# Performance work log

Hardware: AMD Instinct MI355X
Metric: run time of the kernel (lower is better)

## Reference

```python
import jax, jax.numpy as jnp
import numpy as np

N = 100000   # nodes
E = 1600000  # edges (before self-loops)
F = 128      # num_features
H = 128      # hidden_dim
EPS = 1e-5   # BatchNorm eps


def setup_inputs() -> dict:
    key = jax.random.key(0)
    ks = jax.random.split(key, 8)
    x = jax.random.normal(ks[0], (N, F), dtype=jnp.float32)
    edge_index = jax.random.randint(ks[1], (2, E), 0, N, dtype=jnp.int64)

    def lin(k, din, dout):
        s = 1.0 / np.sqrt(din)
        kw, kb = jax.random.split(k)
        W = jax.random.uniform(kw, (din, dout), jnp.float32, -s, s)
        b = jax.random.uniform(kb, (dout,), jnp.float32, -s, s)
        return W, b

    W1, b1 = lin(ks[2], F, H)
    W2, b2 = lin(ks[3], H, H)
    W3, b3 = lin(ks[4], H, H)
    Wc, bc = lin(ks[5], H, 2)

    def bn_params():
        return (jnp.ones((H,), jnp.float32), jnp.zeros((H,), jnp.float32),
                jnp.zeros((H,), jnp.float32), jnp.ones((H,), jnp.float32))

    g1, be1, rm1, rv1 = bn_params()
    g2, be2, rm2, rv2 = bn_params()
    g3, be3, rm3, rv3 = bn_params()

    return {"x": x, "edge_index": edge_index,
            "W1": W1, "b1": b1, "W2": W2, "b2": b2, "W3": W3, "b3": b3,
            "g1": g1, "be1": be1, "rm1": rm1, "rv1": rv1,
            "g2": g2, "be2": be2, "rm2": rm2, "rv2": rv2,
            "g3": g3, "be3": be3, "rm3": rm3, "rv3": rv3,
            "Wc": Wc, "bc": bc}


def _gcn_norm(edge_index, num_nodes):
    # add self-loops, compute symmetric normalization (PyG GCNConv default)
    loop = jnp.arange(num_nodes, dtype=edge_index.dtype)
    src = jnp.concatenate([edge_index[0], loop])
    dst = jnp.concatenate([edge_index[1], loop])
    deg = jax.ops.segment_sum(jnp.ones_like(dst, dtype=jnp.float32), dst,
                              num_segments=num_nodes)
    dinv = jnp.where(deg > 0, jax.lax.rsqrt(deg), 0.0)
    norm = dinv[src] * dinv[dst]  # [E+N]
    return src, dst, norm


def _gcn_conv(x, W, b, src, dst, norm, num_nodes):
    h = x @ W                              # [N, H] linear first
    msg = h[src] * norm[:, None]           # gather + scale  [E+N, H]
    out = jax.ops.segment_sum(msg, dst, num_segments=num_nodes)  # scatter-add
    return out + b


def _bn_eval(x, g, be, rm, rv):
    return (x - rm) * jax.lax.rsqrt(rv + EPS) * g + be


def reference(x, edge_index,
              W1, b1, W2, b2, W3, b3,
              g1, be1, rm1, rv1,
              g2, be2, rm2, rv2,
              g3, be3, rm3, rv3,
              Wc, bc):
    n = x.shape[0]
    src, dst, norm = _gcn_norm(edge_index, n)
    h = _gcn_conv(x, W1, b1, src, dst, norm, n)
    h = _bn_eval(jax.nn.relu(h), g1, be1, rm1, rv1)
    # dropout: identity in eval mode
    h = _gcn_conv(h, W2, b2, src, dst, norm, n)
    h = _bn_eval(jax.nn.relu(h), g2, be2, rm2, rv2)
    h = _gcn_conv(h, W3, b3, src, dst, norm, n)
    h = _bn_eval(jax.nn.relu(h), g3, be3, rm3, rv3)
    return h @ Wc + bc  # [N, 2]
```

## Files before the change

kernel.cpp:

```cpp
#include <hip/hip_runtime.h>
#include <hip/hip_fp16.h>

#define BN_EPS 1e-5f
#define CHUNK 4096
#define BBITS 7

typedef _Float16 half8 __attribute__((ext_vector_type(8)));
typedef float f32x4 __attribute__((ext_vector_type(4)));

__device__ __forceinline__ float4 f4zero() { return make_float4(0.f, 0.f, 0.f, 0.f); }


__global__ __launch_bounds__(256) void k_pack_hist(const float* __restrict__ W1,
                                                   const float* __restrict__ W2,
                                                   const float* __restrict__ W3,
                                                   _Float16* __restrict__ pW,
                                                   const int* __restrict__ dst,
                                                   int* __restrict__ tableT,
                                                   int nA, int nbuck, int e) {
    __shared__ int h[1024];
    int tid = threadIdx.x;
    if (blockIdx.x < 24) {
        int t = blockIdx.x * 256 + tid;
        int wi = t >> 11;
        int tt = t & 2047;
        const float* W = (wi == 0) ? W1 : ((wi == 1) ? W2 : W3);
        int kc = tt >> 9;
        int rem = tt & 511;
        int ct = rem >> 6;
        int lane = rem & 63;
        int q = lane >> 4;
        int col = ct * 16 + (lane & 15);
        half8 hh;
#pragma unroll
        for (int j = 0; j < 8; ++j)
            hh[j] = (_Float16)W[(kc * 32 + q * 8 + j) * 128 + col];
        *(half8*)(pW + (size_t)t * 8) = hh;
        return;
    }
    int blk = blockIdx.x - 24;
    for (int k = tid; k < 1024; k += 256) h[k] = 0;
    __syncthreads();
    int base = blk * CHUNK;
    if (base + CHUNK <= e && (e & 3) == 0) {
        const int4* d4 = (const int4*)(dst + base);
#pragma unroll
        for (int t = 0; t < CHUNK / 1024; ++t) {
            int4 d = d4[t * 256 + tid];
            atomicAdd(&h[d.x >> BBITS], 1);
            atomicAdd(&h[d.y >> BBITS], 1);
            atomicAdd(&h[d.z >> BBITS], 1);
            atomicAdd(&h[d.w >> BBITS], 1);
        }
    } else {
        for (int i = base + tid; i < e && i < base + CHUNK; i += 256)
            atomicAdd(&h[dst[i] >> BBITS], 1);
    }
    __syncthreads();
    for (int k = tid; k < nbuck; k += 256)
        tableT[(size_t)k * nA + blk] = h[k];
}


__global__ __launch_bounds__(1024) void k_scan_block(const int* __restrict__ in,
                                                     int* __restrict__ outp,
                                                     int* __restrict__ partials, int len) {
    __shared__ int s[1024];
    int t = threadIdx.x;
    int gid = blockIdx.x * 1024 + t;
    int v = (gid < len) ? in[gid] : 0;
    int x = v;
    s[t] = x;
    __syncthreads();
    for (int d = 1; d < 1024; d <<= 1) {
        int y = (t >= d) ? s[t - d] : 0;
        __syncthreads();
        x += y;
        s[t] = x;
        __syncthreads();
    }
    if (gid < len) outp[gid] = x - v;
    if (t == 1023) partials[blockIdx.x] = x;
}

__global__ __launch_bounds__(256) void k_scan_addp(int* __restrict__ data,
                                                   const int* __restrict__ partials, int len) {
    __shared__ int red[256];
    int tid = threadIdx.x;
    int K = blockIdx.x >> 2;
    int s = 0;
    for (int t = tid; t < K; t += 256) s += partials[t];
    red[tid] = s;
    __syncthreads();
    for (int d = 128; d > 0; d >>= 1) {
        if (tid < d) red[tid] += red[tid + d];
        __syncthreads();
    }
    int gid = blockIdx.x * 256 + tid;
    if (gid < len) data[gid] += red[0];
}


__global__ __launch_bounds__(256) void k_bucket_scatter(const int* __restrict__ src,
                                                        const int* __restrict__ dst,
                                                        const int* __restrict__ tableT,
                                                        int2* __restrict__ bed,
                                                        int nA, int nbuck, int e) {
    __shared__ int cur[1024];
    int blk = blockIdx.x, tid = threadIdx.x;
    for (int k = tid; k < nbuck; k += 256)
        cur[k] = tableT[(size_t)k * nA + blk];
    __syncthreads();
    int base = blk * CHUNK;
    if (base + CHUNK <= e && (e & 3) == 0) {
        const int4* s4 = (const int4*)(src + base);
        const int4* d4 = (const int4*)(dst + base);
#pragma unroll
        for (int t = 0; t < CHUNK / 1024; ++t) {
            int4 s = s4[t * 256 + tid];
            int4 d = d4[t * 256 + tid];
            int p0 = atomicAdd(&cur[d.x >> BBITS], 1); bed[p0] = make_int2(s.x, d.x);
            int p1 = atomicAdd(&cur[d.y >> BBITS], 1); bed[p1] = make_int2(s.y, d.y);
            int p2 = atomicAdd(&cur[d.z >> BBITS], 1); bed[p2] = make_int2(s.z, d.z);
            int p3 = atomicAdd(&cur[d.w >> BBITS], 1); bed[p3] = make_int2(s.w, d.w);
        }
    } else {
        for (int i = base + tid; i < e && i < base + CHUNK; i += 256) {
            int d = dst[i];
            int p = atomicAdd(&cur[d >> BBITS], 1);
            bed[p] = make_int2(src[i], d);
        }
    }
}


__global__ __launch_bounds__(256) void k_bucket_rank(const int2* __restrict__ bed,
                                                     const int* __restrict__ tableT,
                                                     int* __restrict__ brank,
                                                     int* __restrict__ counts,
                                                     float* __restrict__ dinv,
                                                     int* __restrict__ localOff,
                                                     int* __restrict__ btot,
                                                     int nA, int nbuck, int n, int e) {
    __shared__ int lcnt[128];
    __shared__ int lscan[128];
    int b = blockIdx.x, tid = threadIdx.x;
    if (tid < 128) lcnt[tid] = 0;
    __syncthreads();
    int start = tableT[(size_t)b * nA];
    int end = (b + 1 < nbuck) ? tableT[(size_t)(b + 1) * nA] : e;
    for (int i = start + tid; i < end; i += 256) {
        int2 q = bed[i];
        brank[i] = atomicAdd(&lcnt[q.y & 127], 1);
    }
    __syncthreads();
    int padded = 0;
    if (tid < 128) {
        padded = (lcnt[tid] + 7) & ~7;
        lscan[tid] = padded;
    }
    __syncthreads();
    for (int d = 1; d < 128; d <<= 1) {
        int y = (tid < 128 && tid >= d) ? lscan[tid - d] : 0;
        __syncthreads();
        if (tid < 128) lscan[tid] += y;
        __syncthreads();
    }
    if (tid < 128) {
        int node = (b << BBITS) + tid;
        if (node < n) {
            int c = lcnt[tid];
            counts[node] = c;
            dinv[node] = rsqrtf((float)(c + 1));
            localOff[node] = lscan[tid] - padded;
        }
        if (tid == 127) btot[b] = lscan[127];
    }
}


__global__ __launch_bounds__(1024) void k_scan_buckets(const int* __restrict__ btot,
                                                       int* __restrict__ bucketBase, int nbuck) {
    __shared__ int s[1024];
    int t = threadIdx.x;
    int v = (t < nbuck) ? btot[t] : 0;
    int x = v;
    s[t] = x;
    __syncthreads();
    for (int d = 1; d < 1024; d <<= 1) {
        int y = (t >= d) ? s[t - d] : 0;
        __syncthreads();
        x += y;
        s[t] = x;
        __syncthreads();
    }
    if (t < nbuck) bucketBase[t] = x - v;
    if (t == nbuck - 1) bucketBase[nbuck] = x;
}


__global__ __launch_bounds__(256) void k_finalize(const int* __restrict__ counts,
                                                  const int* __restrict__ localOff,
                                                  const int* __restrict__ bucketBase,
                                                  int* __restrict__ offs,
                                                  int* __restrict__ er,
                                                  const int2* __restrict__ bed,
                                                  const int* __restrict__ brank,
                                                  unsigned int* __restrict__ bufAzero,
                                                  int n, int e, int gN, int nbuck) {
    int tid = threadIdx.x;
    if (blockIdx.x < gN) {
        int node = blockIdx.x * 256 + tid;
        if (node < n) {
            int c = counts[node];
            int o = bucketBase[node >> BBITS] + localOff[node];
            offs[node] = o;
            int pc = (c + 7) & ~7;
            for (int j = c; j < pc; ++j) er[o + j] = n << 8;
        }
        if (node == 0) offs[n] = bucketBase[nbuck];
        if (blockIdx.x == 0 && tid < 64) bufAzero[tid] = 0u;
    } else {
        int i = ((blockIdx.x - gN) * 256 + tid) * 2;
        if (i + 1 < e) {
            int4 q = *(const int4*)(bed + i);
            int2 r = *(const int2*)(brank + i);
            er[bucketBase[q.y >> BBITS] + localOff[q.y] + r.x] = q.x << 8;
            er[bucketBase[q.w >> BBITS] + localOff[q.w] + r.y] = q.z << 8;
        } else if (i < e) {
            int2 q = bed[i];
            er[bucketBase[q.y >> BBITS] + localOff[q.y] + brank[i]] = q.x << 8;
        }
    }
}


template <bool AF32>
__global__ __launch_bounds__(256) void k_gemm_mfma(const void* __restrict__ Av,
                                                   const _Float16* __restrict__ pW,
                                                   const float* __restrict__ dinv,
                                                   uint4* __restrict__ C, int n) {
    __shared__ char smem[32768];
    uint4* sW = (uint4*)smem;
    int tid = threadIdx.x;

    {
        const uint4* gW = (const uint4*)pW;
#pragma unroll
        for (int i = 0; i < 8; ++i) sW[tid + 256 * i] = gW[tid + 256 * i];
    }
    __syncthreads();

    int wave = tid >> 6, lane = tid & 63;
    int quad = lane >> 4, l16 = lane & 15;
    int row0 = blockIdx.x * 64 + wave * 16;
    int arow = row0 + l16;
    int arowc = (arow < n) ? arow : (n - 1);

    half8 af[4];
    if (AF32) {
        const float* A = (const float*)Av + (size_t)arowc * 128 + quad * 8;
#pragma unroll
        for (int kc = 0; kc < 4; ++kc) {
            float4 lo = *(const float4*)(A + kc * 32);
            float4 hi = *(const float4*)(A + kc * 32 + 4);
            half8 h;
            h[0] = (_Float16)lo.x; h[1] = (_Float16)lo.y;
            h[2] = (_Float16)lo.z; h[3] = (_Float16)lo.w;
            h[4] = (_Float16)hi.x; h[5] = (_Float16)hi.y;
            h[6] = (_Float16)hi.z; h[7] = (_Float16)hi.w;
            af[kc] = h;
        }
    } else {
        const _Float16* A = (const _Float16*)Av + (size_t)arowc * 128 + quad * 8;
#pragma unroll
        for (int kc = 0; kc < 4; ++kc)
            af[kc] = *(const half8*)(A + kc * 32);
    }

    f32x4 acc[8];
#pragma unroll
    for (int ct = 0; ct < 8; ++ct) acc[ct] = (f32x4){0.f, 0.f, 0.f, 0.f};

#pragma unroll
    for (int kc = 0; kc < 4; ++kc) {
#pragma unroll
        for (int ct = 0; ct < 8; ++ct) {
            half8 bf = *(half8*)&sW[(kc * 8 + ct) * 64 + lane];
            acc[ct] = __builtin_amdgcn_mfma_f32_16x16x32_f16(af[kc], bf, acc[ct], 0, 0, 0);
        }
    }

    __syncthreads();

    _Float16* eb = (_Float16*)smem + wave * 16 * 136;
    float dv[4];
#pragma unroll
    for (int r = 0; r < 4; ++r) {
        int rr = row0 + quad * 4 + r;
        dv[r] = dinv[(rr < n) ? rr : (n - 1)];
    }
#pragma unroll
    for (int ct = 0; ct < 8; ++ct)
#pragma unroll
        for (int r = 0; r < 4; ++r)
            eb[(quad * 4 + r) * 136 + ct * 16 + l16] = (_Float16)(acc[ct][r] * dv[r]);

#pragma unroll
    for (int i = 0; i < 4; ++i) {
        int linear = i * 64 + lane;
        int r = linear >> 4, c = linear & 15;
        uint4 v = *(uint4*)((char*)eb + r * 272 + c * 16);
        int row = row0 + r;
        if (row < n) C[(size_t)row * 16 + c] = v;
    }
}


__device__ __forceinline__ void acc_row(float4& acc, uint2 q) {
    asm("v_fma_mix_f32 %0, %1, 1.0, %0 op_sel:[0,0,0] op_sel_hi:[1,0,0]" : "+v"(acc.x) : "v"(q.x));
    asm("v_fma_mix_f32 %0, %1, 1.0, %0 op_sel:[1,0,0] op_sel_hi:[1,0,0]" : "+v"(acc.y) : "v"(q.x));
    asm("v_fma_mix_f32 %0, %1, 1.0, %0 op_sel:[0,0,0] op_sel_hi:[1,0,0]" : "+v"(acc.z) : "v"(q.y));
    asm("v_fma_mix_f32 %0, %1, 1.0, %0 op_sel:[1,0,0] op_sel_hi:[1,0,0]" : "+v"(acc.w) : "v"(q.y));
}

template <bool FUSE_CLS>
__global__ __launch_bounds__(256) void k_aggregate(const uint2* __restrict__ Ah,
                                                   const int* __restrict__ offs,
                                                   const int* __restrict__ er,
                                                   const float* __restrict__ dinv,
                                                   const float* __restrict__ bias,
                                                   const float* __restrict__ g,
                                                   const float* __restrict__ be,
                                                   const float* __restrict__ rm,
                                                   const float* __restrict__ rv,
                                                   uint2* __restrict__ Hout,
                                                   const float* __restrict__ Wc,
                                                   const float* __restrict__ bc,
                                                   float* __restrict__ out, int n) {
    int lane = threadIdx.x & 31;
    int node = blockIdx.x * 8 + (threadIdx.x >> 5);
    if (node >= n) return;

    const char* AhB = (const char*)Ah;
    unsigned int l8 = (unsigned int)lane * 8u;

    float4 acc = f4zero();
    acc_row(acc, *(const uint2*)(AhB + (((unsigned int)node << 8) + l8)));

    int e0 = offs[node], e1 = offs[node + 1];
    for (int e = e0; e < e1; e += 8) {
        int4 ra = *(const int4*)(er + e);
        int4 rb = *(const int4*)(er + e + 4);
        uint2 v0 = *(const uint2*)(AhB + ((unsigned int)ra.x + l8));
        uint2 v1 = *(const uint2*)(AhB + ((unsigned int)ra.y + l8));
        uint2 v2 = *(const uint2*)(AhB + ((unsigned int)ra.z + l8));
        uint2 v3 = *(const uint2*)(AhB + ((unsigned int)ra.w + l8));
        uint2 v4 = *(const uint2*)(AhB + ((unsigned int)rb.x + l8));
        uint2 v5 = *(const uint2*)(AhB + ((unsigned int)rb.y + l8));
        uint2 v6 = *(const uint2*)(AhB + ((unsigned int)rb.z + l8));
        uint2 v7 = *(const uint2*)(AhB + ((unsigned int)rb.w + l8));
        acc_row(acc, v0); acc_row(acc, v1); acc_row(acc, v2); acc_row(acc, v3);
        acc_row(acc, v4); acc_row(acc, v5); acc_row(acc, v6); acc_row(acc, v7);
    }

    float di = dinv[node];
    acc.x *= di; acc.y *= di; acc.z *= di; acc.w *= di;

    float4 b4  = ((const float4*)bias)[lane];
    float4 g4  = ((const float4*)g)[lane];
    float4 be4 = ((const float4*)be)[lane];
    float4 rm4 = ((const float4*)rm)[lane];
    float4 rv4 = ((const float4*)rv)[lane];

    float4 o;
    float v;
    v = fmaxf(acc.x + b4.x, 0.f); o.x = (v - rm4.x) * rsqrtf(rv4.x + BN_EPS) * g4.x + be4.x;
    v = fmaxf(acc.y + b4.y, 0.f); o.y = (v - rm4.y) * rsqrtf(rv4.y + BN_EPS) * g4.y + be4.y;
    v = fmaxf(acc.z + b4.z, 0.f); o.z = (v - rm4.z) * rsqrtf(rv4.z + BN_EPS) * g4.z + be4.z;
    v = fmaxf(acc.w + b4.w, 0.f); o.w = (v - rm4.w) * rsqrtf(rv4.w + BN_EPS) * g4.w + be4.w;

    if (!FUSE_CLS) {
        __half2 p0 = __floats2half2_rn(o.x, o.y);
        __half2 p1 = __floats2half2_rn(o.z, o.w);
        uint2 u;
        u.x = *(unsigned int*)&p0;
        u.y = *(unsigned int*)&p1;
        Hout[(size_t)node * 32 + lane] = u;
    } else {
        const float4* Wv = (const float4*)Wc;
        float4 w01 = Wv[2 * lane];
        float4 w23 = Wv[2 * lane + 1];
        float p0 = o.x * w01.x + o.y * w01.z + o.z * w23.x + o.w * w23.z;
        float p1 = o.x * w01.y + o.y * w01.w + o.z * w23.y + o.w * w23.w;
#pragma unroll
        for (int d = 16; d >= 1; d >>= 1) {
            p0 += __shfl_down(p0, d, 32);
            p1 += __shfl_down(p1, d, 32);
        }
        if (lane == 0) {
            out[node * 2 + 0] = p0 + bc[0];
            out[node * 2 + 1] = p1 + bc[1];
        }
    }
}


extern "C" void kernel_launch(void* const* d_in, const int* in_sizes, int n_in,
                              void* d_out, int out_size, void* d_ws, size_t ws_size,
                              hipStream_t stream) {
    const float* x   = (const float*)d_in[0];
    const int*   ei  = (const int*)d_in[1];
    const float* W1  = (const float*)d_in[2];
    const float* b1  = (const float*)d_in[3];
    const float* W2  = (const float*)d_in[4];
    const float* b2  = (const float*)d_in[5];
    const float* W3  = (const float*)d_in[6];
    const float* b3  = (const float*)d_in[7];
    const float* g1  = (const float*)d_in[8];
    const float* be1 = (const float*)d_in[9];
    const float* rm1 = (const float*)d_in[10];
    const float* rv1 = (const float*)d_in[11];
    const float* g2  = (const float*)d_in[12];
    const float* be2 = (const float*)d_in[13];
    const float* rm2 = (const float*)d_in[14];
    const float* rv2 = (const float*)d_in[15];
    const float* g3  = (const float*)d_in[16];
    const float* be3 = (const float*)d_in[17];
    const float* rm3 = (const float*)d_in[18];
    const float* rv3 = (const float*)d_in[19];
    const float* Wc  = (const float*)d_in[20];
    const float* bc  = (const float*)d_in[21];
    float* out = (float*)d_out;

    int n = in_sizes[0] / 128;
    int e = in_sizes[1] / 2;
    const int* src = ei;
    const int* dst = ei + e;

    char* ws = (char*)d_ws;
    size_t off = 0;
    auto alloc = [&](size_t bytes) -> char* {
        char* p = ws + off;
        off += (bytes + 255) & ~(size_t)255;
        return p;
    };
    int nA    = (e + CHUNK - 1) / CHUNK;
    int nbuck = (n + (1 << BBITS) - 1) >> BBITS;
    int tlen  = nbuck * nA;
    int erCap = e + 8 * n;

    char*      bufA     = (char*) alloc((size_t)(n + 1) * 256);
    char*      bufH     = (char*) alloc((size_t)n * 256);
    float*     dinv     = (float*)alloc((size_t)n * 4);
    int*       counts   = (int*)  alloc((size_t)n * 4);
    int*       offs     = (int*)  alloc((size_t)(n + 1) * 4);
    int*       localOff = (int*)  alloc((size_t)n * 4);
    int*       btot     = (int*)  alloc((size_t)(nbuck + 1) * 4);
    int*       bktBase  = (int*)  alloc((size_t)(nbuck + 1) * 4);
    int*       tableT   = (int*)  alloc((size_t)(tlen + 1) * 4);
    int*       parts    = (int*)  alloc(8192);
    int*       er       = (int*)  alloc((size_t)erCap * 4);
    _Float16*  pW       = (_Float16*)alloc(3 * 16384 * 2);
    (void)ws_size; (void)n_in; (void)out_size;

    int2* bed   = (int2*)bufH;
    int*  brank = (int*)(bufH + (size_t)e * 8);

    int gN  = (n + 255) / 256;
    int nbT = (tlen + 1023) / 1024;

    k_pack_hist<<<24 + nA, 256, 0, stream>>>(W1, W2, W3, pW, dst, tableT, nA, nbuck, e);
    k_scan_block<<<nbT, 1024, 0, stream>>>(tableT, tableT, parts, tlen);
    k_scan_addp<<<(tlen + 255) / 256, 256, 0, stream>>>(tableT, parts, tlen);
    k_bucket_scatter<<<nA, 256, 0, stream>>>(src, dst, tableT, bed, nA, nbuck, e);
    k_bucket_rank<<<nbuck, 256, 0, stream>>>(bed, tableT, brank, counts, dinv, localOff,
                                             btot, nA, nbuck, n, e);
    k_scan_buckets<<<1, 1024, 0, stream>>>(btot, bktBase, nbuck);
    int gP = gN + (e / 2 + 255) / 256 + 1;
    k_finalize<<<gP, 256, 0, stream>>>(counts, localOff, bktBase, offs, er, bed, brank,
                                       (unsigned int*)(bufA + (size_t)n * 256), n, e, gN, nbuck);

    int gGemm = (n + 63) / 64;
    int gAgg  = (n + 7) / 8;

    k_gemm_mfma<true><<<gGemm, 256, 0, stream>>>(x, pW, dinv, (uint4*)bufA, n);
    k_aggregate<false><<<gAgg, 256, 0, stream>>>((const uint2*)bufA, offs, er, dinv,
                                                 b1, g1, be1, rm1, rv1, (uint2*)bufH,
                                                 nullptr, nullptr, nullptr, n);

    k_gemm_mfma<false><<<gGemm, 256, 0, stream>>>(bufH, pW + 16384, dinv, (uint4*)bufA, n);
    k_aggregate<false><<<gAgg, 256, 0, stream>>>((const uint2*)bufA, offs, er, dinv,
                                                 b2, g2, be2, rm2, rv2, (uint2*)bufH,
                                                 nullptr, nullptr, nullptr, n);

    k_gemm_mfma<false><<<gGemm, 256, 0, stream>>>(bufH, pW + 32768, dinv, (uint4*)bufA, n);
    k_aggregate<true><<<gAgg, 256, 0, stream>>>((const uint2*)bufA, offs, er, dinv,
                                                b3, g3, be3, rm3, rv3, nullptr,
                                                Wc, bc, out, n);
}
```

Baseline: 395.4 us.

## Fuse bucket scan into first GEMM launch and widen aggregate loads to 16 bytes

The single-block bucket-base scan is merged into the first-layer GEMM launch: block 0 does the scan with 256 threads, each handling a serial chunk, and the remaining blocks run the fp32-input GEMM. This removes one launch and lets the scan overlap with GEMM work. The aggregation kernel now uses 16 lanes per node with 16-byte gathers instead of 32 lanes with 8-byte gathers, so fewer, wider memory requests are issued per edge. The per-thread scan buffer has a fixed size of 8, so it assumes nbuck is at most 2048, and the half-width groups raise register use per thread.

```diff
diff --git a/kernel.cpp b/kernel.cpp
--- a/kernel.cpp
+++ b/kernel.cpp
@@ -179,23 +179,132 @@
 }
 
 
-__global__ __launch_bounds__(1024) void k_scan_buckets(const int* __restrict__ btot,
-                                                       int* __restrict__ bucketBase, int nbuck) {
-    __shared__ int s[1024];
-    int t = threadIdx.x;
-    int v = (t < nbuck) ? btot[t] : 0;
-    int x = v;
-    s[t] = x;
-    __syncthreads();
-    for (int d = 1; d < 1024; d <<= 1) {
-        int y = (t >= d) ? s[t - d] : 0;
-        __syncthreads();
-        x += y;
-        s[t] = x;
-        __syncthreads();
-    }
-    if (t < nbuck) bucketBase[t] = x - v;
-    if (t == nbuck - 1) bucketBase[nbuck] = x;
+template <bool AF32>
+__device__ __forceinline__ void gemm_body(int bid, int tid, char* smem,
+                                          const void* __restrict__ Av,
+                                          const _Float16* __restrict__ pW,
+                                          const float* __restrict__ dinv,
+                                          uint4* __restrict__ C, int n) {
+    uint4* sW = (uint4*)smem;
+    {
+        const uint4* gW = (const uint4*)pW;
+#pragma unroll
+        for (int i = 0; i < 8; ++i) sW[tid + 256 * i] = gW[tid + 256 * i];
+    }
+    __syncthreads();
+
+    int wave = tid >> 6, lane = tid & 63;
+    int quad = lane >> 4, l16 = lane & 15;
+    int row0 = bid * 64 + wave * 16;
+    int arow = row0 + l16;
+    int arowc = (arow < n) ? arow : (n - 1);
+
+    half8 af[4];
+    if (AF32) {
+        const float* A = (const float*)Av + (size_t)arowc * 128 + quad * 8;
+#pragma unroll
+        for (int kc = 0; kc < 4; ++kc) {
+            float4 lo = *(const float4*)(A + kc * 32);
+            float4 hi = *(const float4*)(A + kc * 32 + 4);
+            half8 h;
+            h[0] = (_Float16)lo.x; h[1] = (_Float16)lo.y;
+            h[2] = (_Float16)lo.z; h[3] = (_Float16)lo.w;
+            h[4] = (_Float16)hi.x; h[5] = (_Float16)hi.y;
+            h[6] = (_Float16)hi.z; h[7] = (_Float16)hi.w;
+            af[kc] = h;
+        }
+    } else {
+        const _Float16* A = (const _Float16*)Av + (size_t)arowc * 128 + quad * 8;
+#pragma unroll
+        for (int kc = 0; kc < 4; ++kc)
+            af[kc] = *(const half8*)(A + kc * 32);
+    }
+
+    f32x4 acc[8];
+#pragma unroll
+    for (int ct = 0; ct < 8; ++ct) acc[ct] = (f32x4){0.f, 0.f, 0.f, 0.f};
+
+#pragma unroll
+    for (int kc = 0; kc < 4; ++kc) {
+#pragma unroll
+        for (int ct = 0; ct < 8; ++ct) {
+            half8 bf = *(half8*)&sW[(kc * 8 + ct) * 64 + lane];
+            acc[ct] = __builtin_amdgcn_mfma_f32_16x16x32_f16(af[kc], bf, acc[ct], 0, 0, 0);
+        }
+    }
+
+    __syncthreads();
+
+    _Float16* eb = (_Float16*)smem + wave * 16 * 136;
+    float dv[4];
+#pragma unroll
+    for (int r = 0; r < 4; ++r) {
+        int rr = row0 + quad * 4 + r;
+        dv[r] = dinv[(rr < n) ? rr : (n - 1)];
+    }
+#pragma unroll
+    for (int ct = 0; ct < 8; ++ct)
+#pragma unroll
+        for (int r = 0; r < 4; ++r)
+            eb[(quad * 4 + r) * 136 + ct * 16 + l16] = (_Float16)(acc[ct][r] * dv[r]);
+
+#pragma unroll
+    for (int i = 0; i < 4; ++i) {
+        int linear = i * 64 + lane;
+        int r = linear >> 4, c = linear & 15;
+        uint4 v = *(uint4*)((char*)eb + r * 272 + c * 16);
+        int row = row0 + r;
+        if (row < n) C[(size_t)row * 16 + c] = v;
+    }
+}
+
+__global__ __launch_bounds__(256) void k_gemm_mfma(const void* __restrict__ Av,
+                                                   const _Float16* __restrict__ pW,
+                                                   const float* __restrict__ dinv,
+                                                   uint4* __restrict__ C, int n) {
+    __shared__ char smem[32768];
+    gemm_body<false>(blockIdx.x, threadIdx.x, smem, Av, pW, dinv, C, n);
+}
+
+
+__global__ __launch_bounds__(256) void k_scanb_gemm(const int* __restrict__ btot,
+                                                    int* __restrict__ bucketBase, int nbuck,
+                                                    const float* __restrict__ x,
+                                                    const _Float16* __restrict__ pW,
+                                                    const float* __restrict__ dinv,
+                                                    uint4* __restrict__ C, int n) {
+    __shared__ char smem[32768];
+    int tid = threadIdx.x;
+    if (blockIdx.x > 0) {
+        gemm_body<true>(blockIdx.x - 1, tid, smem, x, pW, dinv, C, n);
+        return;
+    }
+    int* s = (int*)smem;
+    int per = (nbuck + 255) >> 8;
+    int base = tid * per;
+    int loc[8];
+    int sum = 0;
+#pragma unroll 4
+    for (int j = 0; j < per; ++j) {
+        int v = (base + j < nbuck) ? btot[base + j] : 0;
+        loc[j] = sum;
+        sum += v;
+    }
+    int x_ = sum;
+    s[tid] = x_;
+    __syncthreads();
+    for (int d = 1; d < 256; d <<= 1) {
+        int y = (tid >= d) ? s[tid - d] : 0;
+        __syncthreads();
+        x_ += y;
+        s[tid] = x_;
+        __syncthreads();
+    }
+    int off = x_ - sum;
+#pragma unroll 4
+    for (int j = 0; j < per; ++j)
+        if (base + j < nbuck) bucketBase[base + j] = off + loc[j];
+    if (tid == 255) bucketBase[nbuck] = x_;
 }
 
 
@@ -235,97 +344,20 @@
 }
 
 
-template <bool AF32>
-__global__ __launch_bounds__(256) void k_gemm_mfma(const void* __restrict__ Av,
-                                                   const _Float16* __restrict__ pW,
-                                                   const float* __restrict__ dinv,
-                                                   uint4* __restrict__ C, int n) {
-    __shared__ char smem[32768];
-    uint4* sW = (uint4*)smem;
-    int tid = threadIdx.x;
-
-    {
-        const uint4* gW = (const uint4*)pW;
-#pragma unroll
-        for (int i = 0; i < 8; ++i) sW[tid + 256 * i] = gW[tid + 256 * i];
-    }
-    __syncthreads();
-
-    int wave = tid >> 6, lane = tid & 63;
-    int quad = lane >> 4, l16 = lane & 15;
-    int row0 = blockIdx.x * 64 + wave * 16;
-    int arow = row0 + l16;
-    int arowc = (arow < n) ? arow : (n - 1);
-
-    half8 af[4];
-    if (AF32) {
-        const float* A = (const float*)Av + (size_t)arowc * 128 + quad * 8;
-#pragma unroll
-        for (int kc = 0; kc < 4; ++kc) {
-            float4 lo = *(const float4*)(A + kc * 32);
-            float4 hi = *(const float4*)(A + kc * 32 + 4);
-            half8 h;
-            h[0] = (_Float16)lo.x; h[1] = (_Float16)lo.y;
-            h[2] = (_Float16)lo.z; h[3] = (_Float16)lo.w;
-            h[4] = (_Float16)hi.x; h[5] = (_Float16)hi.y;
-            h[6] = (_Float16)hi.z; h[7] = (_Float16)hi.w;
-            af[kc] = h;
-        }
-    } else {
-        const _Float16* A = (const _Float16*)Av + (size_t)arowc * 128 + quad * 8;
-#pragma unroll
-        for (int kc = 0; kc < 4; ++kc)
-            af[kc] = *(const half8*)(A + kc * 32);
-    }
-
-    f32x4 acc[8];
-#pragma unroll
-    for (int ct = 0; ct < 8; ++ct) acc[ct] = (f32x4){0.f, 0.f, 0.f, 0.f};
-
-#pragma unroll
-    for (int kc = 0; kc < 4; ++kc) {
-#pragma unroll
-        for (int ct = 0; ct < 8; ++ct) {
-            half8 bf = *(half8*)&sW[(kc * 8 + ct) * 64 + lane];
-            acc[ct] = __builtin_amdgcn_mfma_f32_16x16x32_f16(af[kc], bf, acc[ct], 0, 0, 0);
-        }
-    }
-
-    __syncthreads();
-
-    _Float16* eb = (_Float16*)smem + wave * 16 * 136;
-    float dv[4];
-#pragma unroll
-    for (int r = 0; r < 4; ++r) {
-        int rr = row0 + quad * 4 + r;
-        dv[r] = dinv[(rr < n) ? rr : (n - 1)];
-    }
-#pragma unroll
-    for (int ct = 0; ct < 8; ++ct)
-#pragma unroll
-        for (int r = 0; r < 4; ++r)
-            eb[(quad * 4 + r) * 136 + ct * 16 + l16] = (_Float16)(acc[ct][r] * dv[r]);
-
-#pragma unroll
-    for (int i = 0; i < 4; ++i) {
-        int linear = i * 64 + lane;
-        int r = linear >> 4, c = linear & 15;
-        uint4 v = *(uint4*)((char*)eb + r * 272 + c * 16);
-        int row = row0 + r;
-        if (row < n) C[(size_t)row * 16 + c] = v;
-    }
-}
-
-
-__device__ __forceinline__ void acc_row(float4& acc, uint2 q) {
-    asm("v_fma_mix_f32 %0, %1, 1.0, %0 op_sel:[0,0,0] op_sel_hi:[1,0,0]" : "+v"(acc.x) : "v"(q.x));
-    asm("v_fma_mix_f32 %0, %1, 1.0, %0 op_sel:[1,0,0] op_sel_hi:[1,0,0]" : "+v"(acc.y) : "v"(q.x));
-    asm("v_fma_mix_f32 %0, %1, 1.0, %0 op_sel:[0,0,0] op_sel_hi:[1,0,0]" : "+v"(acc.z) : "v"(q.y));
-    asm("v_fma_mix_f32 %0, %1, 1.0, %0 op_sel:[1,0,0] op_sel_hi:[1,0,0]" : "+v"(acc.w) : "v"(q.y));
-}
+__device__ __forceinline__ void acc_row4(float4& aL, float4& aH, uint4 q) {
+    asm("v_fma_mix_f32 %0, %1, 1.0, %0 op_sel:[0,0,0] op_sel_hi:[1,0,0]" : "+v"(aL.x) : "v"(q.x));
+    asm("v_fma_mix_f32 %0, %1, 1.0, %0 op_sel:[1,0,0] op_sel_hi:[1,0,0]" : "+v"(aL.y) : "v"(q.x));
+    asm("v_fma_mix_f32 %0, %1, 1.0, %0 op_sel:[0,0,0] op_sel_hi:[1,0,0]" : "+v"(aL.z) : "v"(q.y));
+    asm("v_fma_mix_f32 %0, %1, 1.0, %0 op_sel:[1,0,0] op_sel_hi:[1,0,0]" : "+v"(aL.w) : "v"(q.y));
+    asm("v_fma_mix_f32 %0, %1, 1.0, %0 op_sel:[0,0,0] op_sel_hi:[1,0,0]" : "+v"(aH.x) : "v"(q.z));
+    asm("v_fma_mix_f32 %0, %1, 1.0, %0 op_sel:[1,0,0] op_sel_hi:[1,0,0]" : "+v"(aH.y) : "v"(q.z));
+    asm("v_fma_mix_f32 %0, %1, 1.0, %0 op_sel:[0,0,0] op_sel_hi:[1,0,0]" : "+v"(aH.z) : "v"(q.w));
+    asm("v_fma_mix_f32 %0, %1, 1.0, %0 op_sel:[1,0,0] op_sel_hi:[1,0,0]" : "+v"(aH.w) : "v"(q.w));
+}
+
 
 template <bool FUSE_CLS>
-__global__ __launch_bounds__(256) void k_aggregate(const uint2* __restrict__ Ah,
+__global__ __launch_bounds__(256) void k_aggregate(const uint4* __restrict__ Ah,
                                                    const int* __restrict__ offs,
                                                    const int* __restrict__ er,
                                                    const float* __restrict__ dinv,
@@ -334,69 +366,82 @@
                                                    const float* __restrict__ be,
                                                    const float* __restrict__ rm,
                                                    const float* __restrict__ rv,
-                                                   uint2* __restrict__ Hout,
+                                                   uint4* __restrict__ Hout,
                                                    const float* __restrict__ Wc,
                                                    const float* __restrict__ bc,
                                                    float* __restrict__ out, int n) {
-    int lane = threadIdx.x & 31;
-    int node = blockIdx.x * 8 + (threadIdx.x >> 5);
+    int lane = threadIdx.x & 15;
+    int node = blockIdx.x * 16 + (threadIdx.x >> 4);
     if (node >= n) return;
 
     const char* AhB = (const char*)Ah;
-    unsigned int l8 = (unsigned int)lane * 8u;
-
-    float4 acc = f4zero();
-    acc_row(acc, *(const uint2*)(AhB + (((unsigned int)node << 8) + l8)));
+    unsigned int l16 = (unsigned int)lane * 16u;
+
+    float4 aL = f4zero(), aH = f4zero();
+    acc_row4(aL, aH, *(const uint4*)(AhB + (((unsigned int)node << 8) + l16)));
 
     int e0 = offs[node], e1 = offs[node + 1];
     for (int e = e0; e < e1; e += 8) {
         int4 ra = *(const int4*)(er + e);
         int4 rb = *(const int4*)(er + e + 4);
-        uint2 v0 = *(const uint2*)(AhB + ((unsigned int)ra.x + l8));
-        uint2 v1 = *(const uint2*)(AhB + ((unsigned int)ra.y + l8));
-        uint2 v2 = *(const uint2*)(AhB + ((unsigned int)ra.z + l8));
-        uint2 v3 = *(const uint2*)(AhB + ((unsigned int)ra.w + l8));
-        uint2 v4 = *(const uint2*)(AhB + ((unsigned int)rb.x + l8));
-        uint2 v5 = *(const uint2*)(AhB + ((unsigned int)rb.y + l8));
-        uint2 v6 = *(const uint2*)(AhB + ((unsigned int)rb.z + l8));
-        uint2 v7 = *(const uint2*)(AhB + ((unsigned int)rb.w + l8));
-        acc_row(acc, v0); acc_row(acc, v1); acc_row(acc, v2); acc_row(acc, v3);
-        acc_row(acc, v4); acc_row(acc, v5); acc_row(acc, v6); acc_row(acc, v7);
+        uint4 v0 = *(const uint4*)(AhB + ((unsigned int)ra.x + l16));
+        uint4 v1 = *(const uint4*)(AhB + ((unsigned int)ra.y + l16));
+        uint4 v2 = *(const uint4*)(AhB + ((unsigned int)ra.z + l16));
+        uint4 v3 = *(const uint4*)(AhB + ((unsigned int)ra.w + l16));
+        uint4 v4 = *(const uint4*)(AhB + ((unsigned int)rb.x + l16));
+        uint4 v5 = *(const uint4*)(AhB + ((unsigned int)rb.y + l16));
+        uint4 v6 = *(const uint4*)(AhB + ((unsigned int)rb.z + l16));
+        uint4 v7 = *(const uint4*)(AhB + ((unsigned int)rb.w + l16));
+        acc_row4(aL, aH, v0); acc_row4(aL, aH, v1); acc_row4(aL, aH, v2); acc_row4(aL, aH, v3);
+        acc_row4(aL, aH, v4); acc_row4(aL, aH, v5); acc_row4(aL, aH, v6); acc_row4(aL, aH, v7);
     }
 
     float di = dinv[node];
-    acc.x *= di; acc.y *= di; acc.z *= di; acc.w *= di;
-
-    float4 b4  = ((const float4*)bias)[lane];
-    float4 g4  = ((const float4*)g)[lane];
-    float4 be4 = ((const float4*)be)[lane];
-    float4 rm4 = ((const float4*)rm)[lane];
-    float4 rv4 = ((const float4*)rv)[lane];
-
-    float4 o;
+    aL.x *= di; aL.y *= di; aL.z *= di; aL.w *= di;
+    aH.x *= di; aH.y *= di; aH.z *= di; aH.w *= di;
+
+    float4 bL  = ((const float4*)bias)[2 * lane], bH  = ((const float4*)bias)[2 * lane + 1];
+    float4 gL  = ((const float4*)g)[2 * lane],    gH  = ((const float4*)g)[2 * lane + 1];
+    float4 beL = ((const float4*)be)[2 * lane],   beH = ((const float4*)be)[2 * lane + 1];
+    float4 rmL = ((const float4*)rm)[2 * lane],   rmH = ((const float4*)rm)[2 * lane + 1];
+    float4 rvL = ((const float4*)rv)[2 * lane],   rvH = ((const float4*)rv)[2 * lane + 1];
+
+    float4 oL, oH;
     float v;
-    v = fmaxf(acc.x + b4.x, 0.f); o.x = (v - rm4.x) * rsqrtf(rv4.x + BN_EPS) * g4.x + be4.x;
-    v = fmaxf(acc.y + b4.y, 0.f); o.y = (v - rm4.y) * rsqrtf(rv4.y + BN_EPS) * g4.y + be4.y;
-    v = fmaxf(acc.z + b4.z, 0.f); o.z = (v - rm4.z) * rsqrtf(rv4.z + BN_EPS) * g4.z + be4.z;
-    v = fmaxf(acc.w + b4.w, 0.f); o.w = (v - rm4.w) * rsqrtf(rv4.w + BN_EPS) * g4.w + be4.w;
+    v = fmaxf(aL.x + bL.x, 0.f); oL.x = (v - rmL.x) * rsqrtf(rvL.x + BN_EPS) * gL.x + beL.x;
+    v = fmaxf(aL.y + bL.y, 0.f); oL.y = (v - rmL.y) * rsqrtf(rvL.y + BN_EPS) * gL.y + beL.y;
+    v = fmaxf(aL.z + bL.z, 0.f); oL.z = (v - rmL.z) * rsqrtf(rvL.z + BN_EPS) * gL.z + beL.z;
+    v = fmaxf(aL.w + bL.w, 0.f); oL.w = (v - rmL.w) * rsqrtf(rvL.w + BN_EPS) * gL.w + beL.w;
+    v = fmaxf(aH.x + bH.x, 0.f); oH.x = (v - rmH.x) * rsqrtf(rvH.x + BN_EPS) * gH.x + beH.x;
+    v = fmaxf(aH.y + bH.y, 0.f); oH.y = (v - rmH.y) * rsqrtf(rvH.y + BN_EPS) * gH.y + beH.y;
+    v = fmaxf(aH.z + bH.z, 0.f); oH.z = (v - rmH.z) * rsqrtf(rvH.z + BN_EPS) * gH.z + beH.z;
+    v = fmaxf(aH.w + bH.w, 0.f); oH.w = (v - rmH.w) * rsqrtf(rvH.w + BN_EPS) * gH.w + beH.w;
 
     if (!FUSE_CLS) {
-        __half2 p0 = __floats2half2_rn(o.x, o.y);
-        __half2 p1 = __floats2half2_rn(o.z, o.w);
-        uint2 u;
+        __half2 p0 = __floats2half2_rn(oL.x, oL.y);
+        __half2 p1 = __floats2half2_rn(oL.z, oL.w);
+        __half2 p2 = __floats2half2_rn(oH.x, oH.y);
+        __half2 p3 = __floats2half2_rn(oH.z, oH.w);
+        uint4 u;
         u.x = *(unsigned int*)&p0;
         u.y = *(unsigned int*)&p1;
-        Hout[(size_t)node * 32 + lane] = u;
+        u.z = *(unsigned int*)&p2;
+        u.w = *(unsigned int*)&p3;
+        Hout[(size_t)node * 16 + lane] = u;
     } else {
         const float4* Wv = (const float4*)Wc;
-        float4 w01 = Wv[2 * lane];
-        float4 w23 = Wv[2 * lane + 1];
-        float p0 = o.x * w01.x + o.y * w01.z + o.z * w23.x + o.w * w23.z;
-        float p1 = o.x * w01.y + o.y * w01.w + o.z * w23.y + o.w * w23.w;
-#pragma unroll
-        for (int d = 16; d >= 1; d >>= 1) {
-            p0 += __shfl_down(p0, d, 32);
-            p1 += __shfl_down(p1, d, 32);
+        float4 w0 = Wv[4 * lane];
+        float4 w1 = Wv[4 * lane + 1];
+        float4 w2 = Wv[4 * lane + 2];
+        float4 w3 = Wv[4 * lane + 3];
+        float p0 = oL.x * w0.x + oL.y * w0.z + oL.z * w1.x + oL.w * w1.z
+                 + oH.x * w2.x + oH.y * w2.z + oH.z * w3.x + oH.w * w3.z;
+        float p1 = oL.x * w0.y + oL.y * w0.w + oL.z * w1.y + oL.w * w1.w
+                 + oH.x * w2.y + oH.y * w2.w + oH.z * w3.y + oH.w * w3.w;
+#pragma unroll
+        for (int d = 8; d >= 1; d >>= 1) {
+            p0 += __shfl_down(p0, d, 16);
+            p1 += __shfl_down(p1, d, 16);
         }
         if (lane == 0) {
             out[node * 2 + 0] = p0 + bc[0];
@@ -469,6 +514,8 @@
 
     int gN  = (n + 255) / 256;
     int nbT = (tlen + 1023) / 1024;
+    int gGemm = (n + 63) / 64;
+    int gAgg  = (n + 15) / 16;
 
     k_pack_hist<<<24 + nA, 256, 0, stream>>>(W1, W2, W3, pW, dst, tableT, nA, nbuck, e);
     k_scan_block<<<nbT, 1024, 0, stream>>>(tableT, tableT, parts, tlen);
@@ -476,26 +523,21 @@
     k_bucket_scatter<<<nA, 256, 0, stream>>>(src, dst, tableT, bed, nA, nbuck, e);
     k_bucket_rank<<<nbuck, 256, 0, stream>>>(bed, tableT, brank, counts, dinv, localOff,
                                              btot, nA, nbuck, n, e);
-    k_scan_buckets<<<1, 1024, 0, stream>>>(btot, bktBase, nbuck);
+    k_scanb_gemm<<<1 + gGemm, 256, 0, stream>>>(btot, bktBase, nbuck,
+                                                x, pW, dinv, (uint4*)bufA, n);
     int gP = gN + (e / 2 + 255) / 256 + 1;
     k_finalize<<<gP, 256, 0, stream>>>(counts, localOff, bktBase, offs, er, bed, brank,
                                        (unsigned int*)(bufA + (size_t)n * 256), n, e, gN, nbuck);
 
-    int gGemm = (n + 63) / 64;
-    int gAgg  = (n + 7) / 8;
-
-    k_gemm_mfma<true><<<gGemm, 256, 0, stream>>>(x, pW, dinv, (uint4*)bufA, n);
-    k_aggregate<false><<<gAgg, 256, 0, stream>>>((const uint2*)bufA, offs, er, dinv,
-                                                 b1, g1, be1, rm1, rv1, (uint2*)bufH,
+    k_aggregate<false><<<gAgg, 256, 0, stream>>>((const uint4*)bufA, offs, er, dinv,
+                                                 b1, g1, be1, rm1, rv1, (uint4*)bufH,
                                                  nullptr, nullptr, nullptr, n);
-
-    k_gemm_mfma<false><<<gGemm, 256, 0, stream>>>(bufH, pW + 16384, dinv, (uint4*)bufA, n);
-    k_aggregate<false><<<gAgg, 256, 0, stream>>>((const uint2*)bufA, offs, er, dinv,
-                                                 b2, g2, be2, rm2, rv2, (uint2*)bufH,
+    k_gemm_mfma<<<gGemm, 256, 0, stream>>>(bufH, pW + 16384, dinv, (uint4*)bufA, n);
+    k_aggregate<false><<<gAgg, 256, 0, stream>>>((const uint4*)bufA, offs, er, dinv,
+                                                 b2, g2, be2, rm2, rv2, (uint4*)bufH,
                                                  nullptr, nullptr, nullptr, n);
-
-    k_gemm_mfma<false><<<gGemm, 256, 0, stream>>>(bufH, pW + 32768, dinv, (uint4*)bufA, n);
-    k_aggregate<true><<<gAgg, 256, 0, stream>>>((const uint2*)bufA, offs, er, dinv,
+    k_gemm_mfma<<<gGemm, 256, 0, stream>>>(bufH, pW + 32768, dinv, (uint4*)bufA, n);
+    k_aggregate<true><<<gAgg, 256, 0, stream>>>((const uint4*)bufA, offs, er, dinv,
                                                 b3, g3, be3, rm3, rv3, nullptr,
                                                 Wc, bc, out, n);
 }
```

After: 383.5 us. -3.0%, faster.
